# Kernel optimization log

Hardware: AMD Instinct MI355X
Metric: run time of the kernel (lower is better)

## Reference

```python
import jax, jax.numpy as jnp
import numpy as np

B, T, C, IMG = 16, 1024, 4, 64
HID_C = 16                 # self.c (hidden_dim before *image_size)
H = HID_C * IMG            # 1024 GRU hidden size
IN = C * IMG               # 256 GRU input size
L = 2                      # num_layers


def setup_inputs() -> dict:
    key = jax.random.key(0)
    ks = jax.random.split(key, 10)
    s_in = 1.0 / np.sqrt(H)
    return {
        "x": jax.random.normal(ks[0], (B, T, C, IMG), jnp.float32),
        "h0": jnp.zeros((L, B, H), jnp.float32),
        "w_ih_0": jax.random.normal(ks[1], (3 * H, IN), jnp.float32) * s_in,
        "w_hh_0": jax.random.normal(ks[2], (3 * H, H), jnp.float32) * s_in,
        "b_ih_0": jax.random.normal(ks[3], (3 * H,), jnp.float32) * s_in,
        "b_hh_0": jax.random.normal(ks[4], (3 * H,), jnp.float32) * s_in,
        "w_ih_1": jax.random.normal(ks[5], (3 * H, H), jnp.float32) * s_in,
        "w_hh_1": jax.random.normal(ks[6], (3 * H, H), jnp.float32) * s_in,
        "b_ih_1": jax.random.normal(ks[7], (3 * H,), jnp.float32) * s_in,
        "b_hh_1": jax.random.normal(ks[8], (3 * H,), jnp.float32) * s_in,
    }


def _gru_layer(xs, h0, w_ih, w_hh, b_ih, b_hh):
    # xs: [b,t,in], h0: [b,H]. Precompute input-gate matmuls over all t.
    gx = jnp.einsum("bti,gi->btg", xs, w_ih) + b_ih  # [b,t,3H]

    def step(hprev, gx_t):
        gh = hprev @ w_hh.T + b_hh                   # [b,3H]
        xr, xz, xn = jnp.split(gx_t, 3, axis=-1)
        hr, hz, hn = jnp.split(gh, 3, axis=-1)
        r = jax.nn.sigmoid(xr + hr)
        z = jax.nn.sigmoid(xz + hz)
        n = jnp.tanh(xn + r * hn)
        hnew = (1.0 - z) * n + z * hprev
        return hnew, hnew

    h_last, ys = jax.lax.scan(step, h0, jnp.swapaxes(gx, 0, 1))
    return jnp.swapaxes(ys, 0, 1), h_last            # [b,t,H], [b,H]


def reference(x, h0, w_ih_0, w_hh_0, b_ih_0, b_hh_0,
              w_ih_1, w_hh_1, b_ih_1, b_hh_1):
    b, t, c, h = x.shape
    xs = x.reshape(b, t, c * h)
    y0, h_last0 = _gru_layer(xs, h0[0], w_ih_0, w_hh_0, b_ih_0, b_hh_0)
    y1, h_last1 = _gru_layer(y0, h0[1], w_ih_1, w_hh_1, b_ih_1, b_hh_1)
    y = y1.reshape(b, t, HID_C, h)
    last_states = jnp.stack([h_last0, h_last1], axis=0)  # [L,b,H]
    return y, last_states
```

## Files before the change

### kernel.cpp

```cpp
#include <hip/hip_runtime.h>
#include <stdint.h>

#define T_ 1024

typedef float  floatx4 __attribute__((ext_vector_type(4)));
typedef short  shortx8 __attribute__((ext_vector_type(8)));
typedef unsigned long long u64;

union U16 { u64 q[2]; unsigned d[4]; shortx8 v; };

__device__ __forceinline__ unsigned short f2bf(float f) {
  union { float f; unsigned u; } v; v.f = f;
  return (unsigned short)((v.u + 0x7FFFu + ((v.u >> 16) & 1u)) >> 16);
}
__device__ __forceinline__ unsigned pkbf(float lo, float hi) {
  unsigned r;
  asm("v_cvt_pk_bf16_f32 %0, %1, %2" : "=v"(r) : "v"(lo), "v"(hi));
  return r;
}
__device__ __forceinline__ u64 lda(const u64* p) {
  return __hip_atomic_load(p, __ATOMIC_RELAXED, __HIP_MEMORY_SCOPE_AGENT);
}
__device__ __forceinline__ void sta(u64* p, u64 v) {
  __hip_atomic_store(p, v, __ATOMIC_RELAXED, __HIP_MEMORY_SCOPE_AGENT);
}

__global__ void prep_kernel(uint4* __restrict__ fz) {
  long gid = (long)blockIdx.x * 256 + threadIdx.x;
  if (gid < 98304L) { uint4 z; z.x = z.y = z.z = z.w = 0u; fz[gid] = z; }
}

#define MFMA __builtin_amdgcn_mfma_f32_16x16x32_bf16

template<int L>
__device__ __forceinline__ void gru_wave(int lb, int tid,
    const float* __restrict__ x,
    const float* __restrict__ whh, const float* __restrict__ wih,
    const float* __restrict__ bih, const float* __restrict__ bhh,
    u64* __restrict__ y0buf, u64* __restrict__ h1ring,
    u64* __restrict__ f0, u64* __restrict__ f1,
    float* __restrict__ dout,
    short* __restrict__ wlds, float (*part)[4][4][16][17])
{
  constexpr int KW  = L ? 2048 : 1280;
  constexpr int WS  = KW + 8;
  constexpr int NC  = L ? 8 : 16;
  constexpr int NR  = 3 * NC;
  constexpr int KXs = L ? 1024 : 256;
  const int cb = lb * NC;
  const int w  = tid >> 6;
  const int l  = tid & 63;
  const int lr = l & 15, lq = l >> 4;
  const int c  = L ? (lr & 7) : lr;

  for (int i = tid; i < NR * (KW / 8); i += 256) {
    int row = i / (KW / 8);
    int k   = (i % (KW / 8)) * 8;
    int g = row / NC, cc = row % NC;
    const float* src = (k < 1024) ? (whh + (long)(g * 1024 + cb + cc) * 1024 + k)
                                  : (wih + (long)(g * 1024 + cb + cc) * KXs + (k - 1024));
    float4 a = *(const float4*)src;
    float4 b = *(const float4*)(src + 4);
    uint4 t4;
    t4.x = pkbf(a.x, a.y); t4.y = pkbf(a.z, a.w);
    t4.z = pkbf(b.x, b.y); t4.w = pkbf(b.z, b.w);
    *(uint4*)(wlds + row * WS + k) = t4;
  }

  const int gb = tid >> (L ? 3 : 4);
  const int gc = tid & (NC - 1);
  const bool isg = tid < 16 * NC;
  float bir = 0, biz = 0, bin = 0, bhr = 0, bhz = 0, bhn = 0;
  if (isg) {
    bir = bih[cb + gc];        bhr = bhh[cb + gc];
    biz = bih[1024 + cb + gc]; bhz = bhh[1024 + cb + gc];
    bin = bih[2048 + cb + gc]; bhn = bhh[2048 + cb + gc];
  }
  __syncthreads();

  const short* w0 = wlds + (0 * NC + c) * WS;
  const short* w1 = wlds + (1 * NC + c) * WS;
  const short* w2 = wlds + (2 * NC + c) * WS;

  float hp = 0.f;

  for (int t = 0; t < T_; ++t) {
    floatx4 ar = {0.f, 0.f, 0.f, 0.f};
    floatx4 az = ar, anh = ar, anx = ar;

    if constexpr (L == 0) {
#pragma unroll
      for (int j = 0; j < 2; ++j) {
        const int kt = w * 2 + j;
        const float* xs = x + (long)lr * 262144 + (long)t * 256 + kt * 32 + lq * 8;
        float4 a = *(const float4*)xs;
        float4 b = *(const float4*)(xs + 4);
        U16 u;
        u.d[0] = pkbf(a.x, a.y); u.d[1] = pkbf(a.z, a.w);
        u.d[2] = pkbf(b.x, b.y); u.d[3] = pkbf(b.z, b.w);
        const int ko = 1024 + kt * 32 + lq * 8;
        ar  = MFMA(u.v, *(const shortx8*)(w0 + ko), ar,  0, 0, 0);
        az  = MFMA(u.v, *(const shortx8*)(w1 + ko), az,  0, 0, 0);
        anx = MFMA(u.v, *(const shortx8*)(w2 + ko), anx, 0, 0, 0);
      }
      if (t > 0) {
        const u64* fp = f0 + (long)(t - 1) * 64 + l;
        for (;;) {
          u64 fl = lda(fp);
          if (__all(fl != 0)) break;
          __builtin_amdgcn_s_sleep(1);
        }
        const u64* base = y0buf + ((long)(t - 1) * 16 + lr) * 256 + w * 64 + lq * 2;
        u64 q[16];
#pragma unroll
        for (int j = 0; j < 8; ++j) {
          q[2 * j]     = lda(base + j * 8);
          q[2 * j + 1] = lda(base + j * 8 + 1);
        }
#pragma unroll
        for (int j = 0; j < 8; ++j) {
          U16 u; u.q[0] = q[2 * j]; u.q[1] = q[2 * j + 1];
          const int ko = (w * 8 + j) * 32 + lq * 8;
          ar  = MFMA(u.v, *(const shortx8*)(w0 + ko), ar,  0, 0, 0);
          az  = MFMA(u.v, *(const shortx8*)(w1 + ko), az,  0, 0, 0);
          anh = MFMA(u.v, *(const shortx8*)(w2 + ko), anh, 0, 0, 0);
        }
      }
    } else {
      {
        const u64* fy = f0 + (long)t * 64 + l;
        for (;;) {
          u64 fl = lda(fy);
          if (__all(fl != 0)) break;
          __builtin_amdgcn_s_sleep(1);
        }
      }
      const u64* yb = y0buf + ((long)t * 16 + lr) * 256 + w * 64 + lq * 2;
      u64 qy[16], qh[16];
#pragma unroll
      for (int j = 0; j < 8; ++j) {
        qy[2 * j]     = lda(yb + j * 8);
        qy[2 * j + 1] = lda(yb + j * 8 + 1);
      }
      if (t > 0) {
        const u64* fh = f1 + (long)(t - 1) * 128 + l;
        for (;;) {
          u64 a = lda(fh), b = lda(fh + 64);
          if (__all(a != 0 && b != 0)) break;
          __builtin_amdgcn_s_sleep(1);
        }
        const u64* hb = h1ring + ((long)((t - 1) & 7) * 16 + lr) * 256 + w * 64 + lq * 2;
#pragma unroll
        for (int j = 0; j < 8; ++j) {
          qh[2 * j]     = lda(hb + j * 8);
          qh[2 * j + 1] = lda(hb + j * 8 + 1);
        }
      }
#pragma unroll
      for (int j = 0; j < 8; ++j) {
        U16 u; u.q[0] = qy[2 * j]; u.q[1] = qy[2 * j + 1];
        const int ko = 1024 + (w * 8 + j) * 32 + lq * 8;
        ar  = MFMA(u.v, *(const shortx8*)(w0 + ko), ar,  0, 0, 0);
        az  = MFMA(u.v, *(const shortx8*)(w1 + ko), az,  0, 0, 0);
        anx = MFMA(u.v, *(const shortx8*)(w2 + ko), anx, 0, 0, 0);
      }
      if (t > 0) {
#pragma unroll
        for (int j = 0; j < 8; ++j) {
          U16 u; u.q[0] = qh[2 * j]; u.q[1] = qh[2 * j + 1];
          const int ko = (w * 8 + j) * 32 + lq * 8;
          ar  = MFMA(u.v, *(const shortx8*)(w0 + ko), ar,  0, 0, 0);
          az  = MFMA(u.v, *(const shortx8*)(w1 + ko), az,  0, 0, 0);
          anh = MFMA(u.v, *(const shortx8*)(w2 + ko), anh, 0, 0, 0);
        }
      }
    }

    const int par = t & 1;
    if (L == 0 || lr < 8) {
#pragma unroll
      for (int r4 = 0; r4 < 4; ++r4) {
        const int b = lq * 4 + r4;
        part[par][w][0][b][lr] = ar[r4];
        part[par][w][1][b][lr] = az[r4];
        part[par][w][2][b][lr] = anh[r4];
        part[par][w][3][b][lr] = anx[r4];
      }
    }
    __syncthreads();

    float hn = 0.f;
    if (isg) {
      float sr = 0, sz = 0, snh = 0, snx = 0;
#pragma unroll
      for (int ww = 0; ww < 4; ++ww) {
        sr  += part[par][ww][0][gb][gc];
        sz  += part[par][ww][1][gb][gc];
        snh += part[par][ww][2][gb][gc];
        snx += part[par][ww][3][gb][gc];
      }
      float r = 1.f / (1.f + __expf(-(sr + bir + bhr)));
      float z = 1.f / (1.f + __expf(-(sz + biz + bhz)));
      float targ = snx + bin + r * (snh + bhn);
      float e2 = __expf(2.f * targ);
      float n = 1.f - 2.f / (e2 + 1.f);
      hn = (1.f - z) * n + z * hp;
      hp = hn;

      unsigned hv = f2bf(hn);
      unsigned v1 = (unsigned)__shfl_down((int)hv, 1);
      unsigned v2 = (unsigned)__shfl_down((int)hv, 2);
      unsigned v3 = (unsigned)__shfl_down((int)hv, 3);
      if ((gc & 3) == 0) {
        u64 word = (u64)(hv | (v1 << 16)) | ((u64)(v2 | (v3 << 16)) << 32);
        if constexpr (L == 0)
          sta(y0buf + ((long)t * 16 + gb) * 256 + ((cb + gc) >> 2), word);
        else
          sta(h1ring + ((long)(t & 7) * 16 + gb) * 256 + ((cb + gc) >> 2), word);
      }
    }

    asm volatile("s_waitcnt vmcnt(0)" ::: "memory");
    __syncthreads();
    if (tid == 0)
      sta((L ? f1 + (long)t * 128 : f0 + (long)t * 64) + lb, 1ull);

    if (isg) {
      if constexpr (L == 1) {
        unsigned fv = __float_as_uint(hn);
        unsigned f2v = (unsigned)__shfl_down((int)fv, 1);
        if ((gc & 1) == 0)
          *(u64*)(dout + (long)gb * 1048576 + (long)t * 1024 + cb + gc) =
              (u64)fv | ((u64)f2v << 32);
        if (t == T_ - 1)
          dout[16777216L + 16384 + (long)gb * 1024 + cb + gc] = hn;
      } else {
        if (t == T_ - 1)
          dout[16777216L + (long)gb * 1024 + cb + gc] = hn;
      }
    }
  }
}

__global__ __launch_bounds__(256, 1) void gru_kernel(
    const float* __restrict__ x,
    const float* __restrict__ whh0, const float* __restrict__ wih0,
    const float* __restrict__ bih0, const float* __restrict__ bhh0,
    const float* __restrict__ whh1, const float* __restrict__ wih1,
    const float* __restrict__ bih1, const float* __restrict__ bhh1,
    u64* y0buf, u64* h1ring, u64* f0, u64* f1, float* dout)
{
  __shared__ __align__(16) short wlds[48 * 1288];
  __shared__ float part[2][4][4][16][17];
  const int bid = blockIdx.x, tid = threadIdx.x;
  if (bid < 64)
    gru_wave<0>(bid, tid, x, whh0, wih0, bih0, bhh0, y0buf, h1ring, f0, f1, dout, wlds, part);
  else
    gru_wave<1>(bid - 64, tid, x, whh1, wih1, bih1, bhh1, y0buf, h1ring, f0, f1, dout, wlds, part);
}

extern "C" void kernel_launch(void* const* d_in, const int* in_sizes, int n_in,
                              void* d_out, int out_size, void* d_ws, size_t ws_size,
                              hipStream_t stream) {
  (void)in_sizes; (void)n_in; (void)out_size; (void)ws_size;
  const float* x    = (const float*)d_in[0];
  const float* wih0 = (const float*)d_in[2];
  const float* whh0 = (const float*)d_in[3];
  const float* bih0 = (const float*)d_in[4];
  const float* bhh0 = (const float*)d_in[5];
  const float* wih1 = (const float*)d_in[6];
  const float* whh1 = (const float*)d_in[7];
  const float* bih1 = (const float*)d_in[8];
  const float* bhh1 = (const float*)d_in[9];
  char* ws = (char*)d_ws;
  u64* y0buf  = (u64*)(ws + 0L);
  u64* h1ring = (u64*)(ws + 33554432L);
  u64* f0     = (u64*)(ws + 33816576L);
  u64* f1     = (u64*)(ws + 34340864L);
  float* out  = (float*)d_out;

  prep_kernel<<<384, 256, 0, stream>>>((uint4*)f0);
  gru_kernel<<<192, 256, 0, stream>>>(x, whh0, wih0, bih0, bhh0,
                                      whh1, wih1, bih1, bhh1,
                                      y0buf, h1ring, f0, f1, out);
}
```

Before: 5.766 ms.

## Replace per-block completion flag with per-wave 16-bit flags, dropping barrier

Each producer wave now publishes its own 16-bit completion flag inside the block's 64-bit flag word right after its stores drain, so the second __syncthreads and the single-thread flag store go away. Consumers poll only the flag words covering the rows they read and compare them against an all-waves-done pattern. This shortens the per-timestep critical path of the recurrent chain. The price is more fine-grained atomic stores and a tighter assumption about which waves produce which slices.

```diff
diff --git a/kernel.cpp b/kernel.cpp
--- a/kernel.cpp
+++ b/kernel.cpp
@@ -24,6 +24,12 @@
 __device__ __forceinline__ void sta(u64* p, u64 v) {
   __hip_atomic_store(p, v, __ATOMIC_RELAXED, __HIP_MEMORY_SCOPE_AGENT);
 }
+__device__ __forceinline__ void sta16(unsigned short* p, unsigned short v) {
+  __hip_atomic_store(p, v, __ATOMIC_RELAXED, __HIP_MEMORY_SCOPE_AGENT);
+}
+
+#define FL_ALL4 0x0001000100010001ull
+#define FL_LO2  0x00010001u
 
 __global__ void prep_kernel(uint4* __restrict__ fz) {
   long gid = (long)blockIdx.x * 256 + threadIdx.x;
@@ -104,10 +110,10 @@
         anx = MFMA(u.v, *(const shortx8*)(w2 + ko), anx, 0, 0, 0);
       }
       if (t > 0) {
-        const u64* fp = f0 + (long)(t - 1) * 64 + l;
+        const u64* fp = f0 + (long)(t - 1) * 64 + w * 16 + (l & 15);
         for (;;) {
           u64 fl = lda(fp);
-          if (__all(fl != 0)) break;
+          if (__all(fl == FL_ALL4)) break;
           __builtin_amdgcn_s_sleep(1);
         }
         const u64* base = y0buf + ((long)(t - 1) * 16 + lr) * 256 + w * 64 + lq * 2;
@@ -128,10 +134,10 @@
       }
     } else {
       {
-        const u64* fy = f0 + (long)t * 64 + l;
+        const u64* fy = f0 + (long)t * 64 + w * 16 + (l & 15);
         for (;;) {
           u64 fl = lda(fy);
-          if (__all(fl != 0)) break;
+          if (__all(fl == FL_ALL4)) break;
           __builtin_amdgcn_s_sleep(1);
         }
       }
@@ -143,10 +149,10 @@
         qy[2 * j + 1] = lda(yb + j * 8 + 1);
       }
       if (t > 0) {
-        const u64* fh = f1 + (long)(t - 1) * 128 + l;
+        const u64* fh = f1 + (long)(t - 1) * 128 + w * 32 + (l & 31);
         for (;;) {
-          u64 a = lda(fh), b = lda(fh + 64);
-          if (__all(a != 0 && b != 0)) break;
+          u64 fl = lda(fh);
+          if (__all((unsigned)fl == FL_LO2)) break;
           __builtin_amdgcn_s_sleep(1);
         }
         const u64* hb = h1ring + ((long)((t - 1) & 7) * 16 + lr) * 256 + w * 64 + lq * 2;
@@ -189,7 +195,6 @@
     }
     __syncthreads();
 
-    float hn = 0.f;
     if (isg) {
       float sr = 0, sz = 0, snh = 0, snx = 0;
 #pragma unroll
@@ -204,7 +209,7 @@
       float targ = snx + bin + r * (snh + bhn);
       float e2 = __expf(2.f * targ);
       float n = 1.f - 2.f / (e2 + 1.f);
-      hn = (1.f - z) * n + z * hp;
+      float hn = (1.f - z) * n + z * hp;
       hp = hn;
 
       unsigned hv = f2bf(hn);
@@ -218,14 +223,13 @@
         else
           sta(h1ring + ((long)(t & 7) * 16 + gb) * 256 + ((cb + gc) >> 2), word);
       }
-    }
-
-    asm volatile("s_waitcnt vmcnt(0)" ::: "memory");
-    __syncthreads();
-    if (tid == 0)
-      sta((L ? f1 + (long)t * 128 : f0 + (long)t * 64) + lb, 1ull);
-
-    if (isg) {
+      asm volatile("s_waitcnt vmcnt(0)" ::: "memory");
+      if (l == 0) {
+        unsigned short* fw = (unsigned short*)
+            ((L ? f1 + (long)t * 128 : f0 + (long)t * 64) + lb);
+        sta16(fw + w, (unsigned short)1);
+      }
+
       if constexpr (L == 1) {
         unsigned fv = __float_as_uint(hn);
         unsigned f2v = (unsigned)__shfl_down((int)fv, 1);
```

Result: slower. 7.529 ms (+30.6%).
